# Kernel optimization log

Hardware: AMD Instinct MI355X
Metric: run time of the kernel (lower is better)

The kernel has to match this reference:

```python
import jax, jax.numpy as jnp
import numpy as np
import math

N_EMBD = 1024
N_HEAD = 16
HEAD_DIM = N_EMBD // N_HEAD


def setup_inputs() -> dict:
    key = jax.random.key(0)
    k1, k2, k3 = jax.random.split(key, 3)
    x = jax.random.normal(k1, (2, 2048, N_EMBD), dtype=jnp.float32)
    # nn.Linear(n_embd, 3*n_embd, bias=False): weight shape [3*n_embd, n_embd]
    w_qkv = jax.random.normal(k2, (3 * N_EMBD, N_EMBD), dtype=jnp.float32) * (1.0 / math.sqrt(N_EMBD))
    w_proj = jax.random.normal(k3, (N_EMBD, N_EMBD), dtype=jnp.float32) * (1.0 / math.sqrt(N_EMBD))
    return {"x": x, "w_qkv": w_qkv, "w_proj": w_proj}


def reference(x, w_qkv, w_proj):
    bsz, seq_len, channels = x.shape
    n_head, head_dim = N_HEAD, HEAD_DIM
    # qkv projection: x @ W^T -> [b, s, 3c]
    qkv = jnp.einsum('bsc,dc->bsd', x, w_qkv)
    q, k, v = jnp.split(qkv, 3, axis=2)
    # [b, h, s, hd]
    q = q.reshape(bsz, seq_len, n_head, head_dim).transpose(0, 2, 1, 3)
    k = k.reshape(bsz, seq_len, n_head, head_dim).transpose(0, 2, 1, 3)
    v = v.reshape(bsz, seq_len, n_head, head_dim).transpose(0, 2, 1, 3)
    scale = 1.0 / math.sqrt(head_dim)
    att = jnp.einsum('bhqd,bhkd->bhqk', q, k) * scale  # [b,h,s,s]
    causal = jnp.tril(jnp.ones((seq_len, seq_len), dtype=bool))
    att = jnp.where(causal[None, None, :, :], att, -jnp.inf)
    att = jax.nn.softmax(att, axis=-1)
    # dropout p=0.0 -> identity
    y = jnp.einsum('bhqk,bhkd->bhqd', att, v)
    y = y.transpose(0, 2, 1, 3).reshape(bsz, seq_len, channels)
    return jnp.einsum('bsc,dc->bsd', y, w_proj)
```

## Files before the change

kernel.cpp:

```cpp
#include <hip/hip_runtime.h>
#include <hip/hip_bf16.h>

typedef short short8 __attribute__((ext_vector_type(8)));
typedef float f32x4 __attribute__((ext_vector_type(4)));

#define NB   2
#define SEQ  2048
#define CH   1024
#define NH   16
#define HD   64
#define MROWS (NB*SEQ)
#define QSZ  (NB*NH*SEQ*HD)
#define NX   ((size_t)MROWS * CH)
#define NWQ  ((size_t)3 * CH * CH)
#define NWP  ((size_t)CH * CH)

__device__ __forceinline__ f32x4 mfma16(short8 a, short8 b, f32x4 c) {
    return __builtin_amdgcn_mfma_f32_16x16x32_bf16(a, b, c, 0, 0, 0);
}

__device__ __forceinline__ short bf16_of(float f) {
    return __builtin_bit_cast(short, __float2bfloat16(f));
}
__device__ __forceinline__ unsigned int pkbf(float a, float b) {
    return (unsigned int)(unsigned short)bf16_of(a)
         | ((unsigned int)(unsigned short)bf16_of(b) << 16);
}

__device__ __forceinline__ short8 load8(const __hip_bfloat16* p) {
    return *reinterpret_cast<const short8*>(p);
}
__device__ __forceinline__ short8 load8(const float* p) {
    f32x4 a = *reinterpret_cast<const f32x4*>(p);
    f32x4 b = *reinterpret_cast<const f32x4*>(p + 4);
    short8 r;
    r[0] = bf16_of(a[0]); r[1] = bf16_of(a[1]);
    r[2] = bf16_of(a[2]); r[3] = bf16_of(a[3]);
    r[4] = bf16_of(b[0]); r[5] = bf16_of(b[1]);
    r[6] = bf16_of(b[2]); r[7] = bf16_of(b[3]);
    return r;
}

__device__ __forceinline__ void gload_lds16(const void* g, void* l) {
    __builtin_amdgcn_global_load_lds(
        (const __attribute__((address_space(1))) unsigned int*)g,
        (__attribute__((address_space(3))) unsigned int*)l, 16, 0, 0);
}

__global__ void cvt3_kernel(const float* __restrict__ x,
                            const float* __restrict__ wq,
                            const float* __restrict__ wp,
                            __hip_bfloat16* __restrict__ dst) {
    const size_t i = ((size_t)blockIdx.x * 256 + threadIdx.x) * 8;
    const float* src;
    size_t off;
    if (i < NX)            { src = x;  off = i; }
    else if (i < NX + NWQ) { src = wq; off = i - NX; }
    else                   { src = wp; off = i - NX - NWQ; }
    *(short8*)&dst[i] = load8(src + off);
}

template<int EPI>
__global__ __launch_bounds__(256, 3)
void gemm_bt2(const __hip_bfloat16* __restrict__ A,
              const __hip_bfloat16* __restrict__ W,
              int K, int N,
              float* __restrict__ Cout,
              __hip_bfloat16* __restrict__ qp,
              __hip_bfloat16* __restrict__ kp,
              __hip_bfloat16* __restrict__ vtp)
{
    __shared__ alignas(16) __hip_bfloat16 Asm[2][128 * 32];
    __shared__ alignas(16) __hip_bfloat16 Bsm[2][128 * 32];

    const int tid  = threadIdx.x;
    const int lane = tid & 63;
    const int wave = tid >> 6;
    const int wm   = wave >> 1, wn = wave & 1;
    const int l15  = lane & 15, lg = lane >> 4;

    const int flat = blockIdx.y * gridDim.x + blockIdx.x;
    const int k8   = flat & 7;
    const int j    = flat >> 3;
    constexpr int SN = (EPI == 1) ? 12 : 4;
    const int mt = (k8 & 3) * 8 + (j & 7);
    const int nt = (k8 >> 2) * SN + (j >> 3);
    const int m0 = mt * 128;
    const int n0 = nt * 128;

    f32x4 acc[4][4] = {};

    const int srow = lane >> 2;
    const int scol = (lane & 3) * 8;

    auto stage = [&](int buf, int k0) {
        #pragma unroll
        for (int half = 0; half < 2; ++half) {
            const int row = wave * 32 + half * 16;
            gload_lds16(A + (size_t)(m0 + row + srow) * K + k0 + scol,
                        &Asm[buf][row * 32]);
            gload_lds16(W + (size_t)(n0 + row + srow) * K + k0 + scol,
                        &Bsm[buf][row * 32]);
        }
    };

    auto compute = [&](int buf) {
        short8 af[4], bfr[4];
        #pragma unroll
        for (int mi = 0; mi < 4; ++mi)
            af[mi] = *(const short8*)&Asm[buf][(wm * 64 + mi * 16 + l15) * 32 + lg * 8];
        #pragma unroll
        for (int ni = 0; ni < 4; ++ni)
            bfr[ni] = *(const short8*)&Bsm[buf][(wn * 64 + ni * 16 + l15) * 32 + lg * 8];
        #pragma unroll
        for (int mi = 0; mi < 4; ++mi)
            #pragma unroll
            for (int ni = 0; ni < 4; ++ni)
                acc[mi][ni] = mfma16(af[mi], bfr[ni], acc[mi][ni]);
    };

    stage(0, 0);
    int it = 0;
    for (int k0 = 0; k0 < K; k0 += 32, ++it) {
        const int cur = it & 1;
        __syncthreads();
        if (k0 + 32 < K) stage(cur ^ 1, k0 + 32);
        compute(cur);
    }

    #pragma unroll
    for (int mi = 0; mi < 4; ++mi) {
        #pragma unroll
        for (int ni = 0; ni < 4; ++ni) {
            #pragma unroll
            for (int j2 = 0; j2 < 4; ++j2) {
                const int m = m0 + wm * 64 + mi * 16 + lg * 4 + j2;
                const int n = n0 + wn * 64 + ni * 16 + l15;
                if constexpr (EPI == 0) {
                    Cout[(size_t)m * N + n] = acc[mi][ni][j2];
                } else {
                    const int sec = n >> 10;
                    const int c   = n & 1023;
                    const int h   = c >> 6, d = c & 63;
                    const int b   = m >> 11, s = m & 2047;
                    const int bh  = b * NH + h;
                    if (sec == 0) {
                        qp[((size_t)bh * SEQ + s) * HD + d] =
                            __float2bfloat16(acc[mi][ni][j2] * 0.125f);
                    } else if (sec == 1) {
                        kp[((size_t)bh * SEQ + s) * HD + d] =
                            __float2bfloat16(acc[mi][ni][j2]);
                    } else {
                        vtp[((size_t)bh * HD + d) * SEQ + s] =
                            __float2bfloat16(acc[mi][ni][j2]);
                    }
                }
            }
        }
    }
}

template<int EPI, typename TA, typename TW>
__global__ __launch_bounds__(256, 2)
void gemm_bt(const TA* __restrict__ A,
             const TW* __restrict__ W,
             int K, int N,
             float* __restrict__ Cout,
             __hip_bfloat16* __restrict__ qp,
             __hip_bfloat16* __restrict__ kp,
             __hip_bfloat16* __restrict__ vtp)
{
    __shared__ alignas(16) __hip_bfloat16 Asm[128 * 32];
    __shared__ alignas(16) __hip_bfloat16 Bsm[128 * 32];

    const int tid  = threadIdx.x;
    const int lane = tid & 63;
    const int wave = tid >> 6;
    const int wm   = wave >> 1, wn = wave & 1;
    const int l15  = lane & 15, lg = lane >> 4;
    const int m0   = blockIdx.x * 128;
    const int n0   = blockIdx.y * 128;

    f32x4 acc[4][4] = {};

    const int c0 = tid, c1 = tid + 256;
    const int r0 = c0 >> 2, kc0 = (c0 & 3) << 3;
    const int r1 = c1 >> 2, kc1 = (c1 & 3) << 3;
    const TA* a0p = A + (size_t)(m0 + r0) * K + kc0;
    const TA* a1p = A + (size_t)(m0 + r1) * K + kc1;
    const TW* b0p = W + (size_t)(n0 + r0) * K + kc0;
    const TW* b1p = W + (size_t)(n0 + r1) * K + kc1;

    for (int k0 = 0; k0 < K; k0 += 32) {
        short8 av0 = load8(a0p + k0);
        short8 av1 = load8(a1p + k0);
        short8 bv0 = load8(b0p + k0);
        short8 bv1 = load8(b1p + k0);
        __syncthreads();
        *(short8*)&Asm[c0 * 8] = av0;
        *(short8*)&Asm[c1 * 8] = av1;
        *(short8*)&Bsm[c0 * 8] = bv0;
        *(short8*)&Bsm[c1 * 8] = bv1;
        __syncthreads();

        short8 af[4], bfr[4];
        #pragma unroll
        for (int mi = 0; mi < 4; ++mi)
            af[mi] = *(const short8*)&Asm[(wm * 64 + mi * 16 + l15) * 32 + lg * 8];
        #pragma unroll
        for (int ni = 0; ni < 4; ++ni)
            bfr[ni] = *(const short8*)&Bsm[(wn * 64 + ni * 16 + l15) * 32 + lg * 8];
        #pragma unroll
        for (int mi = 0; mi < 4; ++mi)
            #pragma unroll
            for (int ni = 0; ni < 4; ++ni)
                acc[mi][ni] = mfma16(af[mi], bfr[ni], acc[mi][ni]);
    }

    #pragma unroll
    for (int mi = 0; mi < 4; ++mi) {
        #pragma unroll
        for (int ni = 0; ni < 4; ++ni) {
            #pragma unroll
            for (int j = 0; j < 4; ++j) {
                const int m = m0 + wm * 64 + mi * 16 + lg * 4 + j;
                const int n = n0 + wn * 64 + ni * 16 + l15;
                if constexpr (EPI == 0) {
                    Cout[(size_t)m * N + n] = acc[mi][ni][j];
                } else {
                    const int sec = n >> 10;
                    const int c   = n & 1023;
                    const int h   = c >> 6, d = c & 63;
                    const int b   = m >> 11, s = m & 2047;
                    const int bh  = b * NH + h;
                    if (sec == 0) {
                        qp[((size_t)bh * SEQ + s) * HD + d] =
                            __float2bfloat16(acc[mi][ni][j] * 0.125f);
                    } else if (sec == 1) {
                        kp[((size_t)bh * SEQ + s) * HD + d] =
                            __float2bfloat16(acc[mi][ni][j]);
                    } else {
                        vtp[((size_t)bh * HD + d) * SEQ + s] =
                            __float2bfloat16(acc[mi][ni][j]);
                    }
                }
            }
        }
    }
}

__global__ __launch_bounds__(256, 3)
void attn_fwd5(const __hip_bfloat16* __restrict__ qp,
               const __hip_bfloat16* __restrict__ kp,
               const __hip_bfloat16* __restrict__ vtp,
               __hip_bfloat16* __restrict__ yp)
{
    __shared__ alignas(16) __hip_bfloat16 Ksm[2][64 * 64];
    __shared__ alignas(16) __hip_bfloat16 Vsm[2][64 * 64];
    __shared__ alignas(16) unsigned int Pw[4][16 * 36];

    const int tid  = threadIdx.x;
    const int lane = tid & 63, wave = tid >> 6;
    const int l15  = lane & 15, lg = lane >> 4;
    const int id   = blockIdx.x;
    const int c    = 31 - (id >> 5);
    const int bh   = id & 31;
    const int b    = bh >> 4, h = bh & 15;
    const int q0   = c * 64 + wave * 16;

    const __hip_bfloat16* Q  = qp  + (size_t)bh * SEQ * HD;
    const __hip_bfloat16* Kp = kp  + (size_t)bh * SEQ * HD;
    const __hip_bfloat16* Vt = vtp + (size_t)bh * HD * SEQ;

    short8 qf[2];
    #pragma unroll
    for (int dk = 0; dk < 2; ++dk)
        qf[dk] = *(const short8*)&Q[(size_t)(q0 + l15) * HD + dk * 32 + lg * 8];

    const short ONE = 0x3F80;
    short8 ones;
    #pragma unroll
    for (int i = 0; i < 8; ++i) ones[i] = ONE;

    f32x4 o[4] = {};
    f32x4 accl = {};
    float m_r = -1e30f;

    auto stage = [&](int buf, int t) {
        const int kv0 = t * 64;
        #pragma unroll
        for (int j = 0; j < 2; ++j) {
            const int ch  = j * 256 + tid;
            const int row = ch >> 3, cb = ch & 7;
            const int cbs = cb ^ (row & 7);
            gload_lds16(Kp + (size_t)(kv0 + row) * HD + cbs * 8,
                        &Ksm[buf][(j * 256 + wave * 64) * 8]);
            gload_lds16(Vt + (size_t)row * SEQ + kv0 + cbs * 8,
                        &Vsm[buf][(j * 256 + wave * 64) * 8]);
        }
    };

    auto compute = [&](int buf, int t) {
        const int kv0 = t * 64;
        f32x4 s[4] = {};
        #pragma unroll
        for (int kf = 0; kf < 4; ++kf)
            #pragma unroll
            for (int dk = 0; dk < 2; ++dk) {
                short8 kfrag = *(const short8*)
                    &Ksm[buf][(kf * 16 + l15) * 64 + (((dk * 4 + lg) ^ (l15 & 7)) * 8)];
                s[kf] = mfma16(kfrag, qf[dk], s[kf]);
            }

        float v[4][4];
        const bool diag = (t == c);
        const int qrow = q0 + l15;
        #pragma unroll
        for (int kf = 0; kf < 4; ++kf)
            #pragma unroll
            for (int j = 0; j < 4; ++j) {
                float sv = s[kf][j];
                if (diag && (kv0 + kf * 16 + lg * 4 + j > qrow)) sv = -1e30f;
                v[kf][j] = sv;
            }
        float mxv = v[0][0];
        #pragma unroll
        for (int kf = 0; kf < 4; ++kf)
            #pragma unroll
            for (int j = 0; j < 4; ++j)
                mxv = fmaxf(mxv, v[kf][j]);
        mxv = fmaxf(mxv, __shfl_xor(mxv, 16));
        mxv = fmaxf(mxv, __shfl_xor(mxv, 32));

        if (__any(mxv > m_r + 8.0f)) {
            const float mn = fmaxf(m_r, mxv);
            const float r  = __expf(m_r - mn);
            m_r = mn;
            float rj[4];
            #pragma unroll
            for (int j = 0; j < 4; ++j)
                rj[j] = __shfl(r, lg * 4 + j);
            #pragma unroll
            for (int j = 0; j < 4; ++j) {
                accl[j] *= rj[j];
                #pragma unroll
                for (int dt = 0; dt < 4; ++dt) o[dt][j] *= rj[j];
            }
        }

        #pragma unroll
        for (int kf = 0; kf < 4; ++kf)
            #pragma unroll
            for (int j = 0; j < 4; ++j)
                v[kf][j] = __expf(v[kf][j] - m_r);

        unsigned int* myP = &Pw[wave][0];
        const int pb = l15 * 36 + lg * 2;
        #pragma unroll
        for (int kf = 0; kf < 4; ++kf) {
            myP[pb + kf * 8]     = pkbf(v[kf][0], v[kf][1]);
            myP[pb + kf * 8 + 1] = pkbf(v[kf][2], v[kf][3]);
        }
        asm volatile("s_waitcnt lgkmcnt(0)" ::: "memory");
        __builtin_amdgcn_sched_barrier(0);
        short8 pa0 = *(const short8*)&Pw[wave][l15 * 36 + lg * 4];
        short8 pa1 = *(const short8*)&Pw[wave][l15 * 36 + 16 + lg * 4];

        accl = mfma16(pa0, ones, accl);
        accl = mfma16(pa1, ones, accl);

        #pragma unroll
        for (int dt = 0; dt < 4; ++dt) {
            short8 vf0 = *(const short8*)
                &Vsm[buf][(dt * 16 + l15) * 64 + (((0 + lg) ^ (l15 & 7)) * 8)];
            short8 vf1 = *(const short8*)
                &Vsm[buf][(dt * 16 + l15) * 64 + (((4 + lg) ^ (l15 & 7)) * 8)];
            o[dt] = mfma16(pa0, vf0, o[dt]);
            o[dt] = mfma16(pa1, vf1, o[dt]);
        }
    };

    stage(0, 0);
    for (int t = 0; t <= c; ++t) {
        const int cur = t & 1;
        __syncthreads();
        if (t < c) stage(cur ^ 1, t + 1);
        compute(cur, t);
    }

    #pragma unroll
    for (int j = 0; j < 4; ++j) {
        const float inv_l = 1.0f / accl[j];
        const int s = q0 + lg * 4 + j;
        #pragma unroll
        for (int dt = 0; dt < 4; ++dt) {
            yp[((size_t)(b * SEQ + s)) * CH + h * 64 + dt * 16 + l15] =
                __float2bfloat16(o[dt][j] * inv_l);
        }
    }
}

extern "C" void kernel_launch(void* const* d_in, const int* in_sizes, int n_in,
                              void* d_out, int out_size, void* d_ws, size_t ws_size,
                              hipStream_t stream)
{
    const float* x      = (const float*)d_in[0];
    const float* w_qkv  = (const float*)d_in[1];
    const float* w_proj = (const float*)d_in[2];
    float* out = (float*)d_out;

    __hip_bfloat16* ws = (__hip_bfloat16*)d_ws;

    if (ws_size >= 41943040ull) {
        __hip_bfloat16* xb   = ws;
        __hip_bfloat16* wqb  = ws + NX;
        __hip_bfloat16* wpb  = ws + NX + NWQ;
        __hip_bfloat16* q_ws = ws + NX + NWQ + NWP;
        __hip_bfloat16* k_ws = q_ws + (size_t)QSZ;
        __hip_bfloat16* vt_ws= k_ws + (size_t)QSZ;
        __hip_bfloat16* y_ws = xb;

        cvt3_kernel<<<(NX + NWQ + NWP) / 2048, 256, 0, stream>>>(x, w_qkv, w_proj, ws);

        gemm_bt2<1><<<dim3(MROWS / 128, 3072 / 128), 256, 0, stream>>>(
            xb, wqb, CH, 3 * CH, nullptr, q_ws, k_ws, vt_ws);

        attn_fwd5<<<1024, 256, 0, stream>>>(q_ws, k_ws, vt_ws, y_ws);

        gemm_bt2<0><<<dim3(MROWS / 128, CH / 128), 256, 0, stream>>>(
            y_ws, wpb, CH, CH, out, nullptr, nullptr, nullptr);
    } else {
        __hip_bfloat16* q_ws  = ws;
        __hip_bfloat16* k_ws  = ws + (size_t)QSZ;
        __hip_bfloat16* vt_ws = ws + (size_t)2 * QSZ;
        __hip_bfloat16* y_ws  = ws + (size_t)3 * QSZ;

        gemm_bt<1, float, float><<<dim3(MROWS / 128, 3072 / 128), 256, 0, stream>>>(
            x, w_qkv, CH, 3 * CH, nullptr, q_ws, k_ws, vt_ws);

        attn_fwd5<<<1024, 256, 0, stream>>>(q_ws, k_ws, vt_ws, y_ws);

        gemm_bt<0, __hip_bfloat16, float><<<dim3(MROWS / 128, CH / 128), 256, 0, stream>>>(
            y_ws, w_proj, CH, CH, out, nullptr, nullptr, nullptr);
    }
}
```

Before: 121.1 us.

## Use 256x256-tile QKV GEMM and remap attention blocks for XCD locality

Adds a gemm_big kernel with 256x256 output tiles, 512 threads and an 8x4 MFMA tile per wave, and uses it for the QKV projection to raise data reuse per LDS load. The grid shrinks to 192 blocks, which may underfill the 256 CUs. The swizzled tile mapping in gemm_bt2 is dropped in favour of plain blockIdx order. Attention blocks are remapped so each XCD handles a contiguous group of batch-heads for L2 locality.

```diff
diff --git a/kernel.cpp b/kernel.cpp
--- a/kernel.cpp
+++ b/kernel.cpp
@@ -58,6 +58,99 @@
     else if (i < NX + NWQ) { src = wq; off = i - NX; }
     else                   { src = wp; off = i - NX - NWQ; }
     *(short8*)&dst[i] = load8(src + off);
+}
+
+template<int EPI>
+__global__ __launch_bounds__(512, 2)
+void gemm_big(const __hip_bfloat16* __restrict__ A,
+              const __hip_bfloat16* __restrict__ W,
+              int K, int N,
+              float* __restrict__ Cout,
+              __hip_bfloat16* __restrict__ qp,
+              __hip_bfloat16* __restrict__ kp,
+              __hip_bfloat16* __restrict__ vtp)
+{
+    __shared__ alignas(16) __hip_bfloat16 Asm[2][256 * 32];
+    __shared__ alignas(16) __hip_bfloat16 Bsm[2][256 * 32];
+
+    const int tid  = threadIdx.x;
+    const int lane = tid & 63;
+    const int wave = tid >> 6;
+    const int wm   = wave >> 2, wn = wave & 3;
+    const int l15  = lane & 15, lg = lane >> 4;
+    const int m0   = blockIdx.x * 256;
+    const int n0   = blockIdx.y * 256;
+
+    f32x4 acc[8][4] = {};
+
+    const int srow = lane >> 2;
+    const int scol = (lane & 3) * 8;
+
+    auto stage = [&](int buf, int k0) {
+        #pragma unroll
+        for (int j = 0; j < 2; ++j) {
+            const int row = j * 128 + wave * 16;
+            gload_lds16(A + (size_t)(m0 + row + srow) * K + k0 + scol,
+                        &Asm[buf][row * 32]);
+            gload_lds16(W + (size_t)(n0 + row + srow) * K + k0 + scol,
+                        &Bsm[buf][row * 32]);
+        }
+    };
+
+    auto compute = [&](int buf) {
+        short8 af[8], bfr[4];
+        #pragma unroll
+        for (int mi = 0; mi < 8; ++mi)
+            af[mi] = *(const short8*)&Asm[buf][(wm * 128 + mi * 16 + l15) * 32 + lg * 8];
+        #pragma unroll
+        for (int ni = 0; ni < 4; ++ni)
+            bfr[ni] = *(const short8*)&Bsm[buf][(wn * 64 + ni * 16 + l15) * 32 + lg * 8];
+        #pragma unroll
+        for (int mi = 0; mi < 8; ++mi)
+            #pragma unroll
+            for (int ni = 0; ni < 4; ++ni)
+                acc[mi][ni] = mfma16(af[mi], bfr[ni], acc[mi][ni]);
+    };
+
+    stage(0, 0);
+    int it = 0;
+    for (int k0 = 0; k0 < K; k0 += 32, ++it) {
+        const int cur = it & 1;
+        __syncthreads();
+        if (k0 + 32 < K) stage(cur ^ 1, k0 + 32);
+        compute(cur);
+    }
+
+    #pragma unroll
+    for (int mi = 0; mi < 8; ++mi) {
+        #pragma unroll
+        for (int ni = 0; ni < 4; ++ni) {
+            #pragma unroll
+            for (int j2 = 0; j2 < 4; ++j2) {
+                const int m = m0 + wm * 128 + mi * 16 + lg * 4 + j2;
+                const int n = n0 + wn * 64 + ni * 16 + l15;
+                if constexpr (EPI == 0) {
+                    Cout[(size_t)m * N + n] = acc[mi][ni][j2];
+                } else {
+                    const int sec = n >> 10;
+                    const int c   = n & 1023;
+                    const int h   = c >> 6, d = c & 63;
+                    const int b   = m >> 11, s = m & 2047;
+                    const int bh  = b * NH + h;
+                    if (sec == 0) {
+                        qp[((size_t)bh * SEQ + s) * HD + d] =
+                            __float2bfloat16(acc[mi][ni][j2] * 0.125f);
+                    } else if (sec == 1) {
+                        kp[((size_t)bh * SEQ + s) * HD + d] =
+                            __float2bfloat16(acc[mi][ni][j2]);
+                    } else {
+                        vtp[((size_t)bh * HD + d) * SEQ + s] =
+                            __float2bfloat16(acc[mi][ni][j2]);
+                    }
+                }
+            }
+        }
+    }
 }
 
 template<int EPI>
@@ -78,15 +171,8 @@
     const int wave = tid >> 6;
     const int wm   = wave >> 1, wn = wave & 1;
     const int l15  = lane & 15, lg = lane >> 4;
-
-    const int flat = blockIdx.y * gridDim.x + blockIdx.x;
-    const int k8   = flat & 7;
-    const int j    = flat >> 3;
-    constexpr int SN = (EPI == 1) ? 12 : 4;
-    const int mt = (k8 & 3) * 8 + (j & 7);
-    const int nt = (k8 >> 2) * SN + (j >> 3);
-    const int m0 = mt * 128;
-    const int n0 = nt * 128;
+    const int m0   = blockIdx.x * 128;
+    const int n0   = blockIdx.y * 128;
 
     f32x4 acc[4][4] = {};
 
@@ -263,8 +349,9 @@
     const int lane = tid & 63, wave = tid >> 6;
     const int l15  = lane & 15, lg = lane >> 4;
     const int id   = blockIdx.x;
-    const int c    = 31 - (id >> 5);
-    const int bh   = id & 31;
+    const int xcd  = id & 7, rest = id >> 3;
+    const int bh   = xcd * 4 + (rest & 3);
+    const int c    = 31 - (rest >> 2);
     const int b    = bh >> 4, h = bh & 15;
     const int q0   = c * 64 + wave * 16;
 
@@ -422,7 +509,7 @@
 
         cvt3_kernel<<<(NX + NWQ + NWP) / 2048, 256, 0, stream>>>(x, w_qkv, w_proj, ws);
 
-        gemm_bt2<1><<<dim3(MROWS / 128, 3072 / 128), 256, 0, stream>>>(
+        gemm_big<1><<<dim3(MROWS / 256, 3072 / 256), 512, 0, stream>>>(
             xb, wqb, CH, 3 * CH, nullptr, q_ws, k_ws, vt_ws);
 
         attn_fwd5<<<1024, 256, 0, stream>>>(q_ws, k_ws, vt_ws, y_ws);
```

After: 144.8 us. 1.2x slower.

## Store GEMM operands in K-tiled layout and remap attention blocks per XCD

Applied to the files above, without the earlier changes.

The conversion kernel now writes x, w_qkv and w_proj in a K-tiled layout ([K/32][rows][32]). Each 128x32 stage tile in the GEMM is then one contiguous chunk instead of 128 strided rows. The attention kernel writes y in the same tiled layout for the projection GEMM and maps block ids so that each XCD handles 4 heads, for better L2 locality. The GEMM's previous L2-aware block swizzle is removed in favour of a plain grid mapping, which may lose some of the cache reuse it provided. The tiled stores in cvt and the attention epilogue may also scatter writes and make them less coalesced.

```diff
diff --git a/kernel.cpp b/kernel.cpp
--- a/kernel.cpp
+++ b/kernel.cpp
@@ -50,14 +50,28 @@
 __global__ void cvt3_kernel(const float* __restrict__ x,
                             const float* __restrict__ wq,
                             const float* __restrict__ wp,
-                            __hip_bfloat16* __restrict__ dst) {
+                            __hip_bfloat16* __restrict__ xb,
+                            __hip_bfloat16* __restrict__ wqb,
+                            __hip_bfloat16* __restrict__ wpb) {
     const size_t i = ((size_t)blockIdx.x * 256 + threadIdx.x) * 8;
     const float* src;
-    size_t off;
-    if (i < NX)            { src = x;  off = i; }
-    else if (i < NX + NWQ) { src = wq; off = i - NX; }
-    else                   { src = wp; off = i - NX - NWQ; }
-    *(short8*)&dst[i] = load8(src + off);
+    __hip_bfloat16* dst;
+    if (i < NX) {
+        const size_t m = i >> 10, k = i & 1023;
+        src = x + i;
+        dst = xb + (k >> 5) * ((size_t)MROWS * 32) + m * 32 + (k & 31);
+    } else if (i < NX + NWQ) {
+        const size_t j = i - NX;
+        const size_t n = j >> 10, k = j & 1023;
+        src = wq + j;
+        dst = wqb + (k >> 5) * ((size_t)3072 * 32) + n * 32 + (k & 31);
+    } else {
+        const size_t j = i - NX - NWQ;
+        const size_t n = j >> 10, k = j & 1023;
+        src = wp + j;
+        dst = wpb + (k >> 5) * ((size_t)1024 * 32) + n * 32 + (k & 31);
+    }
+    *(short8*)dst = load8(src);
 }
 
 template<int EPI>
@@ -78,15 +92,8 @@
     const int wave = tid >> 6;
     const int wm   = wave >> 1, wn = wave & 1;
     const int l15  = lane & 15, lg = lane >> 4;
-
-    const int flat = blockIdx.y * gridDim.x + blockIdx.x;
-    const int k8   = flat & 7;
-    const int j    = flat >> 3;
-    constexpr int SN = (EPI == 1) ? 12 : 4;
-    const int mt = (k8 & 3) * 8 + (j & 7);
-    const int nt = (k8 >> 2) * SN + (j >> 3);
-    const int m0 = mt * 128;
-    const int n0 = nt * 128;
+    const int m0   = blockIdx.x * 128;
+    const int n0   = blockIdx.y * 128;
 
     f32x4 acc[4][4] = {};
 
@@ -94,12 +101,14 @@
     const int scol = (lane & 3) * 8;
 
     auto stage = [&](int buf, int k0) {
+        const size_t ktA = (size_t)(k0 >> 5) * ((size_t)MROWS * 32);
+        const size_t ktW = (size_t)(k0 >> 5) * ((size_t)N * 32);
         #pragma unroll
         for (int half = 0; half < 2; ++half) {
             const int row = wave * 32 + half * 16;
-            gload_lds16(A + (size_t)(m0 + row + srow) * K + k0 + scol,
+            gload_lds16(A + ktA + (size_t)(m0 + row + srow) * 32 + scol,
                         &Asm[buf][row * 32]);
-            gload_lds16(W + (size_t)(n0 + row + srow) * K + k0 + scol,
+            gload_lds16(W + ktW + (size_t)(n0 + row + srow) * 32 + scol,
                         &Bsm[buf][row * 32]);
         }
     };
@@ -249,6 +258,7 @@
     }
 }
 
+template<int TILED>
 __global__ __launch_bounds__(256, 3)
 void attn_fwd5(const __hip_bfloat16* __restrict__ qp,
                const __hip_bfloat16* __restrict__ kp,
@@ -263,8 +273,9 @@
     const int lane = tid & 63, wave = tid >> 6;
     const int l15  = lane & 15, lg = lane >> 4;
     const int id   = blockIdx.x;
-    const int c    = 31 - (id >> 5);
-    const int bh   = id & 31;
+    const int xcd  = id & 7, rest = id >> 3;
+    const int bh   = xcd * 4 + (rest & 3);
+    const int c    = 31 - (rest >> 2);
     const int b    = bh >> 4, h = bh & 15;
     const int q0   = c * 64 + wave * 16;
 
@@ -392,10 +403,17 @@
     for (int j = 0; j < 4; ++j) {
         const float inv_l = 1.0f / accl[j];
         const int s = q0 + lg * 4 + j;
+        const int m = b * SEQ + s;
         #pragma unroll
         for (int dt = 0; dt < 4; ++dt) {
-            yp[((size_t)(b * SEQ + s)) * CH + h * 64 + dt * 16 + l15] =
-                __float2bfloat16(o[dt][j] * inv_l);
+            const int col = h * 64 + dt * 16 + l15;
+            const __hip_bfloat16 hv = __float2bfloat16(o[dt][j] * inv_l);
+            if constexpr (TILED) {
+                yp[(size_t)(col >> 5) * ((size_t)MROWS * 32)
+                   + (size_t)m * 32 + (col & 31)] = hv;
+            } else {
+                yp[(size_t)m * CH + col] = hv;
+            }
         }
     }
 }
@@ -420,12 +438,13 @@
         __hip_bfloat16* vt_ws= k_ws + (size_t)QSZ;
         __hip_bfloat16* y_ws = xb;
 
-        cvt3_kernel<<<(NX + NWQ + NWP) / 2048, 256, 0, stream>>>(x, w_qkv, w_proj, ws);
+        cvt3_kernel<<<(NX + NWQ + NWP) / 2048, 256, 0, stream>>>(
+            x, w_qkv, w_proj, xb, wqb, wpb);
 
         gemm_bt2<1><<<dim3(MROWS / 128, 3072 / 128), 256, 0, stream>>>(
             xb, wqb, CH, 3 * CH, nullptr, q_ws, k_ws, vt_ws);
 
-        attn_fwd5<<<1024, 256, 0, stream>>>(q_ws, k_ws, vt_ws, y_ws);
+        attn_fwd5<1><<<1024, 256, 0, stream>>>(q_ws, k_ws, vt_ws, y_ws);
 
         gemm_bt2<0><<<dim3(MROWS / 128, CH / 128), 256, 0, stream>>>(
             y_ws, wpb, CH, CH, out, nullptr, nullptr, nullptr);
@@ -438,7 +457,7 @@
         gemm_bt<1, float, float><<<dim3(MROWS / 128, 3072 / 128), 256, 0, stream>>>(
             x, w_qkv, CH, 3 * CH, nullptr, q_ws, k_ws, vt_ws);
 
-        attn_fwd5<<<1024, 256, 0, stream>>>(q_ws, k_ws, vt_ws, y_ws);
+        attn_fwd5<0><<<1024, 256, 0, stream>>>(q_ws, k_ws, vt_ws, y_ws);
 
         gemm_bt<0, __hip_bfloat16, float><<<dim3(MROWS / 128, CH / 128), 256, 0, stream>>>(
             y_ws, w_proj, CH, CH, out, nullptr, nullptr, nullptr);
```

Result: faster. 115.1 us (-4.9%).
